# Performance work log

Measured on AMD Instinct MI355X. Metric: run time of the kernel, lower is better.

## Reference

```python
import jax, jax.numpy as jnp
import numpy as np

NUM_CLASSES = 4      # config.class_num (malaria stages)
N = 2048             # total nodes = source + target samples
S = 1024             # source_length
FEAT_IN = 25088      # VGG19 include_top=False -> 7*7*512 flattened
D_FC = 512           # Dense(512)
D_G1 = 512           # config.features_dim (GCNConv1 out)
D_G2 = 256           # config.GCN_hidderlayer_dim_num (GCNConv2 out)


def setup_inputs() -> dict:
    key = jax.random.key(0)
    ks = jax.random.split(key, 8)
    sc = lambda fan_in: np.float32(1.0 / np.sqrt(fan_in))
    return {
        "x": jax.random.normal(ks[0], (N, FEAT_IN), jnp.float32),
        "W_fc": jax.random.normal(ks[1], (FEAT_IN, D_FC), jnp.float32) * sc(FEAT_IN),
        "b_fc": jnp.zeros((D_FC,), jnp.float32),
        "W_g1": jax.random.normal(ks[2], (D_FC, D_G1), jnp.float32) * sc(D_FC),
        "b_g1": jnp.zeros((D_G1,), jnp.float32),
        "W_g2": jax.random.normal(ks[3], (D_G1, D_G2), jnp.float32) * sc(D_G1),
        "b_g2": jnp.zeros((D_G2,), jnp.float32),
        "source_labels": jax.random.randint(ks[4], (S,), 0, NUM_CLASSES),
        "source_length": S,
    }


def reference(x, W_fc, b_fc, W_g1, b_g1, W_g2, b_g2, source_labels, source_length):
    # fc after (omitted frozen) VGG19 backbone + flatten
    feats = x @ W_fc + b_fc                                   # [N, 512]

    # get_centers: per-class SUM of source features (no averaging, faithful)
    src = feats[:source_length]                               # [S, 512]
    centers = jax.ops.segment_sum(src, source_labels, num_segments=NUM_CLASSES)  # [C, 512]

    # per-target euclidean distance to each centroid + argmin
    # (argmin of squared distance == argmin of euclidean distance)
    tgt = feats[source_length:]                               # [T, 512]
    d2 = (jnp.sum(tgt * tgt, axis=1, keepdims=True)
          - 2.0 * (tgt @ centers.T)
          + jnp.sum(centers * centers, axis=1)[None, :])      # [T, C]
    target_labels = jnp.argmin(d2, axis=1)                    # [T] int

    # label-cluster graph: edge iff same label; source block forced to identity
    all_labels = jnp.concatenate([source_labels.astype(jnp.int32),
                                  target_labels.astype(jnp.int32)])
    adj = (all_labels[:, None] == all_labels[None, :]).astype(feats.dtype)  # [N, N]
    adj = adj.at[:source_length, :source_length].set(
        jnp.eye(source_length, dtype=feats.dtype))

    # add_self_loops(value=1) then symmetric gcn_filter D^-1/2 A D^-1/2
    A = adj + jnp.eye(N, dtype=feats.dtype)
    dinv = jax.lax.rsqrt(jnp.sum(A, axis=1))                  # [N]
    A_norm = dinv[:, None] * A * dinv[None, :]                # [N, N]

    # two GCN layers (spektral GCNConv: A_norm @ (X @ W) + b) with relu
    h = jax.nn.relu(A_norm @ (feats @ W_g1) + b_g1)           # [N, 512]
    h = jax.nn.relu(A_norm @ (h @ W_g2) + b_g2)               # [N, 256]
    return (h, A_norm, feats)
```

## Files before the change

kernel.cpp:

```cpp
#include <hip/hip_runtime.h>

#define NROWS 2048
#define SLEN  1024
#define FEAT  25088
#define DFC   512
#define DG1   512
#define DG2   256
#define CSPLIT 128

typedef __attribute__((ext_vector_type(8))) short short8;
typedef __attribute__((ext_vector_type(4))) float f32x4;

__device__ __forceinline__ unsigned short bfbits(float f) {
  unsigned int u = __float_as_uint(f);
  u += 0x7fffu + ((u >> 16) & 1u);
  return (unsigned short)(u >> 16);
}

__device__ __forceinline__ unsigned int cvtpk(float lo, float hi) {
  unsigned int r;
  asm("v_cvt_pk_bf16_f32 %0, %1, %2" : "=v"(r) : "v"(lo), "v"(hi));
  return r;
}

__device__ __forceinline__ void load_lds16(const void* g, void* l) {
  __builtin_amdgcn_global_load_lds(
      (const __attribute__((address_space(1))) unsigned int*)g,
      (__attribute__((address_space(3))) unsigned int*)l, 16, 0, 0);
}

__global__ void transpose_cvt_k(const float* __restrict__ src, unsigned short* __restrict__ dst,
                                int K, int Ncol) {
  __shared__ float tile[64][65];
  int kb = blockIdx.x * 64, nb = blockIdx.y * 64;
  int tx = threadIdx.x & 63, ty = threadIdx.x >> 6;
  #pragma unroll
  for (int i = ty; i < 64; i += 4)
    tile[i][tx] = src[(size_t)(kb + i) * Ncol + (nb + tx)];
  __syncthreads();
  #pragma unroll
  for (int i = ty; i < 64; i += 4)
    dst[(size_t)(nb + i) * K + (kb + tx)] = bfbits(tile[tx][i]);
}

template<bool AF32>
__global__ __launch_bounds__(256) void gemm_k(const void* __restrict__ Aptr,
    const unsigned short* __restrict__ BT, float* __restrict__ Cacc,
    int K, int Ncols, int tiles_n, int ksteps) {
  __shared__ unsigned short Al[2][128 * 64];
  __shared__ unsigned short Bl[2][128 * 64];
  int tid = threadIdx.x;
  int m0 = (blockIdx.x / tiles_n) * 128;
  int n0 = (blockIdx.x % tiles_n) * 128;
  int kbase = blockIdx.y * ksteps * 64;
  int wid = tid >> 6, lane = tid & 63;
  int wm = wid >> 1, wn = wid & 1;
  int lrow = lane & 15, lko = lane >> 4;

  f32x4 acc[4][4];
  #pragma unroll
  for (int i = 0; i < 4; i++)
    #pragma unroll
    for (int j = 0; j < 4; j++) acc[i][j] = (f32x4){0.f, 0.f, 0.f, 0.f};

  float4 pa[8];

  auto loadA_regs = [&](int k0) {
    const float* A = (const float*)Aptr;
    #pragma unroll
    for (int j = 0; j < 4; j++) {
      int ch = tid + j * 256;
      int r = ch >> 3, c = ch & 7;
      const float* g = A + (size_t)(m0 + r) * K + k0 + c * 8;
      pa[2 * j]     = *reinterpret_cast<const float4*>(g);
      pa[2 * j + 1] = *reinterpret_cast<const float4*>(g + 4);
    }
  };
  auto cvtWriteA = [&](int buf) {
    #pragma unroll
    for (int j = 0; j < 4; j++) {
      int ch = tid + j * 256;
      int r = ch >> 3, c = ch & 7;
      int p = c ^ (r & 7);
      int4 o;
      o.x = (int)cvtpk(pa[2 * j].x,     pa[2 * j].y);
      o.y = (int)cvtpk(pa[2 * j].z,     pa[2 * j].w);
      o.z = (int)cvtpk(pa[2 * j + 1].x, pa[2 * j + 1].y);
      o.w = (int)cvtpk(pa[2 * j + 1].z, pa[2 * j + 1].w);
      *reinterpret_cast<int4*>((char*)Al[buf] + r * 128 + p * 16) = o;
    }
  };
  auto stageA_lds = [&](int buf, int k0) {
    const unsigned short* A = (const unsigned short*)Aptr;
    #pragma unroll
    for (int j = 0; j < 4; j++) {
      int chb = j * 256 + wid * 64;
      int ch = chb + lane;
      int r = ch >> 3, c = (ch & 7) ^ (r & 7);
      load_lds16(A + (size_t)(m0 + r) * K + k0 + c * 8, (char*)Al[buf] + chb * 16);
    }
  };
  auto stageB = [&](int buf, int k0) {
    #pragma unroll
    for (int j = 0; j < 4; j++) {
      int chb = j * 256 + wid * 64;
      int ch = chb + lane;
      int r = ch >> 3, c = (ch & 7) ^ (r & 7);
      load_lds16(BT + (size_t)(n0 + r) * K + k0 + c * 8, (char*)Bl[buf] + chb * 16);
    }
  };

  if constexpr (AF32) { loadA_regs(kbase); cvtWriteA(0); }
  else                { stageA_lds(0, kbase); }
  stageB(0, kbase);
  __syncthreads();

  int cur = 0;
  for (int t = 0; t < ksteps; ++t) {
    int k1 = kbase + (t + 1) * 64;
    bool more = (t + 1 < ksteps);
    if (more) {
      if constexpr (AF32) loadA_regs(k1);
      else                stageA_lds(cur ^ 1, k1);
      stageB(cur ^ 1, k1);
    }
    #pragma unroll
    for (int kk = 0; kk < 2; kk++) {
      short8 af[4], bfv[4];
      #pragma unroll
      for (int mi = 0; mi < 4; mi++) {
        int R = wm * 64 + mi * 16 + lrow;
        int slot = ((kk << 2) | lko) ^ (lrow & 7);
        af[mi] = *reinterpret_cast<const short8*>((char*)Al[cur] + R * 128 + slot * 16);
      }
      #pragma unroll
      for (int ni = 0; ni < 4; ni++) {
        int R = wn * 64 + ni * 16 + lrow;
        int slot = ((kk << 2) | lko) ^ (lrow & 7);
        bfv[ni] = *reinterpret_cast<const short8*>((char*)Bl[cur] + R * 128 + slot * 16);
      }
      #pragma unroll
      for (int mi = 0; mi < 4; mi++)
        #pragma unroll
        for (int ni = 0; ni < 4; ni++)
          acc[mi][ni] = __builtin_amdgcn_mfma_f32_16x16x32_bf16(af[mi], bfv[ni], acc[mi][ni], 0, 0, 0);
    }
    if constexpr (AF32) { if (more) cvtWriteA(cur ^ 1); }
    __syncthreads();
    cur ^= 1;
  }

  #pragma unroll
  for (int mi = 0; mi < 4; mi++)
    #pragma unroll
    for (int ni = 0; ni < 4; ni++)
      #pragma unroll
      for (int r = 0; r < 4; r++) {
        int row = m0 + wm * 64 + mi * 16 + lko * 4 + r;
        int col = n0 + wn * 64 + ni * 16 + lrow;
        atomicAdd(&Cacc[(size_t)row * Ncols + col], acc[mi][ni][r]);
      }
}

__global__ void feats_fin_k(const float* __restrict__ facc, const float* __restrict__ bfc,
                            float* __restrict__ outf, unsigned short* __restrict__ outbf) {
  int i = blockIdx.y;
  int n = blockIdx.x * 256 + threadIdx.x;
  float v = facc[(size_t)i * DFC + n] + bfc[n];
  outf[(size_t)i * DFC + n] = v;
  outbf[(size_t)i * DFC + n] = bfbits(v);
}

__global__ void seg_sum_part_k(const float* __restrict__ x, const int* __restrict__ slab,
                               float* __restrict__ sxp) {
  int k4 = blockIdx.x * 256 + threadIdx.x;
  if (k4 >= FEAT / 4) return;
  int k = k4 * 4;
  int i0 = blockIdx.y * 64, i1 = i0 + 64;
  float4 a0 = {0,0,0,0}, a1 = {0,0,0,0}, a2 = {0,0,0,0}, a3 = {0,0,0,0};
  #pragma unroll 4
  for (int i = i0; i < i1; i++) {
    float4 v = *reinterpret_cast<const float4*>(x + (size_t)i * FEAT + k);
    int c = slab[i];
    float m0 = (c == 0) ? 1.f : 0.f, m1 = (c == 1) ? 1.f : 0.f;
    float m2 = (c == 2) ? 1.f : 0.f, m3 = (c == 3) ? 1.f : 0.f;
    a0.x += m0 * v.x; a0.y += m0 * v.y; a0.z += m0 * v.z; a0.w += m0 * v.w;
    a1.x += m1 * v.x; a1.y += m1 * v.y; a1.z += m1 * v.z; a1.w += m1 * v.w;
    a2.x += m2 * v.x; a2.y += m2 * v.y; a2.z += m2 * v.z; a2.w += m2 * v.w;
    a3.x += m3 * v.x; a3.y += m3 * v.y; a3.z += m3 * v.z; a3.w += m3 * v.w;
  }
  size_t base = (size_t)blockIdx.y * 4 * FEAT;
  *reinterpret_cast<float4*>(sxp + base + 0 * FEAT + k) = a0;
  *reinterpret_cast<float4*>(sxp + base + 1 * FEAT + k) = a1;
  *reinterpret_cast<float4*>(sxp + base + 2 * FEAT + k) = a2;
  *reinterpret_cast<float4*>(sxp + base + 3 * FEAT + k) = a3;
}

__global__ void seg_sum_reduce_k(const float* __restrict__ sxp, float* __restrict__ sx) {
  int k4 = blockIdx.x * 256 + threadIdx.x;
  if (k4 >= FEAT / 4) return;
  int k = k4 * 4;
  int c = blockIdx.y;
  double s0 = 0, s1 = 0, s2 = 0, s3 = 0;
  #pragma unroll
  for (int p = 0; p < 16; p++) {
    float4 v = *reinterpret_cast<const float4*>(sxp + ((size_t)p * 4 + c) * FEAT + k);
    s0 += (double)v.x; s1 += (double)v.y; s2 += (double)v.z; s3 += (double)v.w;
  }
  float4 r; r.x = (float)s0; r.y = (float)s1; r.z = (float)s2; r.w = (float)s3;
  *reinterpret_cast<float4*>(sx + (size_t)c * FEAT + k) = r;
}

__global__ void count_src_k(const int* __restrict__ slab, int* __restrict__ cnt) {
  __shared__ int c[4];
  if (threadIdx.x < 4) c[threadIdx.x] = 0;
  __syncthreads();
  for (int i = threadIdx.x; i < SLEN; i += 256) atomicAdd(&c[slab[i]], 1);
  __syncthreads();
  if (threadIdx.x < 4) cnt[threadIdx.x] = c[threadIdx.x];
}

__global__ void centers_part_k(const float* __restrict__ sx, const float* __restrict__ W,
                               double* __restrict__ cpart) {
  int n = blockIdx.x * 64 + (threadIdx.x & 63);
  int cc = threadIdx.x >> 6;
  int kb = blockIdx.y * (FEAT / CSPLIT), ke = kb + FEAT / CSPLIT;
  const float* sr = sx + (size_t)cc * FEAT;
  double acc = 0.0;
  #pragma unroll 4
  for (int k = kb; k < ke; k++)
    acc += (double)sr[k] * (double)W[(size_t)k * DFC + n];
  cpart[((size_t)blockIdx.y * 4 + cc) * DFC + n] = acc;
}

__global__ void centers_reduce_k(const double* __restrict__ cpart, const float* __restrict__ bfc,
                                 const int* __restrict__ cntsrc, float* __restrict__ Cent) {
  int idx = blockIdx.x * 256 + threadIdx.x;
  int cc = idx >> 9, n = idx & 511;
  double s = 0.0;
  #pragma unroll 4
  for (int p = 0; p < CSPLIT; p++) s += cpart[((size_t)p * 4 + cc) * DFC + n];
  Cent[idx] = (float)(s + (double)cntsrc[cc] * (double)bfc[n]);
}

__global__ void wc_k(const float* __restrict__ W, const float* __restrict__ Cent,
                     float* __restrict__ wc) {
  __shared__ float cs[4 * DFC];
  for (int i = threadIdx.x; i < 4 * DFC; i += 256) cs[i] = Cent[i];
  __syncthreads();
  int k = blockIdx.x * 256 + threadIdx.x;
  if (k >= FEAT) return;
  const float* wr = W + (size_t)k * DFC;
  double a0 = 0, a1 = 0, a2 = 0, a3 = 0;
  #pragma unroll 2
  for (int n = 0; n < DFC; n += 4) {
    float4 w4 = *reinterpret_cast<const float4*>(wr + n);
    a0 += (double)w4.x * cs[0 * DFC + n] + (double)w4.y * cs[0 * DFC + n + 1]
        + (double)w4.z * cs[0 * DFC + n + 2] + (double)w4.w * cs[0 * DFC + n + 3];
    a1 += (double)w4.x * cs[1 * DFC + n] + (double)w4.y * cs[1 * DFC + n + 1]
        + (double)w4.z * cs[1 * DFC + n + 2] + (double)w4.w * cs[1 * DFC + n + 3];
    a2 += (double)w4.x * cs[2 * DFC + n] + (double)w4.y * cs[2 * DFC + n + 1]
        + (double)w4.z * cs[2 * DFC + n + 2] + (double)w4.w * cs[2 * DFC + n + 3];
    a3 += (double)w4.x * cs[3 * DFC + n] + (double)w4.y * cs[3 * DFC + n + 1]
        + (double)w4.z * cs[3 * DFC + n + 2] + (double)w4.w * cs[3 * DFC + n + 3];
  }
  float4 r; r.x = (float)a0; r.y = (float)a1; r.z = (float)a2; r.w = (float)a3;
  *reinterpret_cast<float4*>(wc + 4 * (size_t)k) = r;
}

__global__ void kj_k(const float* __restrict__ Cent, const float* __restrict__ bfc,
                     float* __restrict__ Kj) {
  int j = threadIdx.x >> 6, lane = threadIdx.x & 63;
  float cn = 0.f, bc = 0.f;
  for (int n = lane; n < DFC; n += 64) {
    float c = Cent[j * DFC + n];
    cn += c * c; bc += bfc[n] * c;
  }
  #pragma unroll
  for (int m = 32; m >= 1; m >>= 1) { cn += __shfl_xor(cn, m); bc += __shfl_xor(bc, m); }
  if (lane == 0) Kj[j] = cn - 2.f * bc;
}

__global__ void d2_labels_k(const float* __restrict__ x, const float* __restrict__ wc,
                            const float* __restrict__ Kj, int* __restrict__ tlab) {
  int row = blockIdx.x;
  int tid = threadIdx.x;
  const float* xr = x + (size_t)(SLEN + row) * FEAT;
  double a0 = 0, a1 = 0, a2 = 0, a3 = 0;
  #pragma unroll 2
  for (int k = tid; k < FEAT; k += 256) {
    float xv = xr[k];
    float4 w4 = *reinterpret_cast<const float4*>(wc + 4 * (size_t)k);
    a0 += (double)xv * w4.x; a1 += (double)xv * w4.y;
    a2 += (double)xv * w4.z; a3 += (double)xv * w4.w;
  }
  #pragma unroll
  for (int m = 32; m >= 1; m >>= 1) {
    a0 += __shfl_xor(a0, m); a1 += __shfl_xor(a1, m);
    a2 += __shfl_xor(a2, m); a3 += __shfl_xor(a3, m);
  }
  __shared__ double s[4][4];
  int wid = tid >> 6, lane = tid & 63;
  if (lane == 0) { s[wid][0] = a0; s[wid][1] = a1; s[wid][2] = a2; s[wid][3] = a3; }
  __syncthreads();
  if (tid == 0) {
    double t0 = s[0][0] + s[1][0] + s[2][0] + s[3][0];
    double t1 = s[0][1] + s[1][1] + s[2][1] + s[3][1];
    double t2 = s[0][2] + s[1][2] + s[2][2] + s[3][2];
    double t3 = s[0][3] + s[1][3] + s[2][3] + s[3][3];
    double s0 = (double)Kj[0] - 2.0 * t0;
    double s1 = (double)Kj[1] - 2.0 * t1;
    double s2 = (double)Kj[2] - 2.0 * t2;
    double s3 = (double)Kj[3] - 2.0 * t3;
    int bi = 0; double b = s0;
    if (s1 < b) { b = s1; bi = 1; }
    if (s2 < b) { b = s2; bi = 2; }
    if (s3 < b) { b = s3; bi = 3; }
    tlab[row] = bi;
  }
}

__global__ void finalize_labels_k(const int* __restrict__ slab, const int* __restrict__ tlab,
                                  const int* __restrict__ cntsrc, int* __restrict__ alllab,
                                  float* __restrict__ dinv) {
  __shared__ int ct[4];
  if (threadIdx.x < 4) ct[threadIdx.x] = 0;
  __syncthreads();
  for (int i = threadIdx.x; i < SLEN; i += 256) atomicAdd(&ct[tlab[i]], 1);
  __syncthreads();
  for (int i = threadIdx.x; i < NROWS; i += 256) {
    int lab = (i < SLEN) ? slab[i] : tlab[i - SLEN];
    alllab[i] = lab;
    float rs = (i < SLEN) ? (2.f + (float)ct[lab])
                          : (1.f + (float)cntsrc[lab] + (float)ct[lab]);
    dinv[i] = 1.f / sqrtf(rs);
  }
}

__global__ void anorm_k(const int* __restrict__ alllab, const float* __restrict__ dinv,
                        float* __restrict__ Aout) {
  int i = blockIdx.y;
  int j0 = (blockIdx.x * 256 + threadIdx.x) * 4;
  int li = alllab[i];
  float di = dinv[i];
  int4 lj = *reinterpret_cast<const int4*>(alllab + j0);
  float4 dj = *reinterpret_cast<const float4*>(dinv + j0);
  int jj[4] = {lj.x, lj.y, lj.z, lj.w};
  float dd[4] = {dj.x, dj.y, dj.z, dj.w};
  float4 o;
  float* op = &o.x;
  #pragma unroll
  for (int e = 0; e < 4; e++) {
    int j = j0 + e;
    float v;
    if (i == j) v = 2.f * di * dd[e];
    else if (i < SLEN && j < SLEN) v = 0.f;
    else v = (li == jj[e]) ? di * dd[e] : 0.f;
    op[e] = v;
  }
  *reinterpret_cast<float4*>(Aout + (size_t)i * NROWS + j0) = o;
}

__global__ void reduce_st_k(const float* __restrict__ Xacc, const int* __restrict__ alllab,
                            const float* __restrict__ dinv, float* __restrict__ ST, int D) {
  int n = blockIdx.x * 256 + threadIdx.x;
  int i0 = blockIdx.y * 32, i1 = i0 + 32;
  float s[4] = {0, 0, 0, 0}, tt[4] = {0, 0, 0, 0};
  for (int i = i0; i < i1; ++i) {
    float v = dinv[i] * Xacc[(size_t)i * D + n];
    int lab = alllab[i];
    bool src = i < SLEN;
    #pragma unroll
    for (int c = 0; c < 4; c++) {
      s[c]  += (src && lab == c) ? v : 0.f;
      tt[c] += (!src && lab == c) ? v : 0.f;
    }
  }
  #pragma unroll
  for (int c = 0; c < 4; c++) {
    atomicAdd(&ST[c * D + n], s[c]);
    atomicAdd(&ST[(4 + c) * D + n], tt[c]);
  }
}

__global__ void apply_prop_k(const float* __restrict__ Xacc, const float* __restrict__ ST,
                             const int* __restrict__ alllab, const float* __restrict__ dinv,
                             const float* __restrict__ bias, float* __restrict__ outf,
                             unsigned short* __restrict__ outbf, int D) {
  int i = blockIdx.y;
  int n = blockIdx.x * 256 + threadIdx.x;
  float dv = dinv[i];
  int lab = alllab[i];
  float xv = Xacc[(size_t)i * D + n];
  float z;
  if (i < SLEN) z = dv * (2.f * dv * xv + ST[(4 + lab) * D + n]);
  else          z = dv * (ST[lab * D + n] + ST[(4 + lab) * D + n] + dv * xv);
  z += bias[n];
  z = fmaxf(z, 0.f);
  if (outf)  outf[(size_t)i * D + n] = z;
  if (outbf) outbf[(size_t)i * D + n] = bfbits(z);
}

extern "C" void kernel_launch(void* const* d_in, const int* in_sizes, int n_in,
                              void* d_out, int out_size, void* d_ws, size_t ws_size,
                              hipStream_t stream) {
  const float* x    = (const float*)d_in[0];
  const float* Wfc  = (const float*)d_in[1];
  const float* bfc  = (const float*)d_in[2];
  const float* Wg1  = (const float*)d_in[3];
  const float* bg1  = (const float*)d_in[4];
  const float* Wg2  = (const float*)d_in[5];
  const float* bg2  = (const float*)d_in[6];
  const int*   slab = (const int*)d_in[7];

  float* out = (float*)d_out;
  float* out_h = out;
  float* out_A = out + 524288;
  float* out_f = out + 4718592;

  char* w = (char*)d_ws;
  unsigned short* wT   = (unsigned short*)(w);
  unsigned short* g1T  = (unsigned short*)(w + 25690112);
  unsigned short* g2T  = (unsigned short*)(w + 26214400);
  float* facc          = (float*)(w + 26476544);
  unsigned short* fbf  = (unsigned short*)(w + 30670848);
  float* x1acc         = (float*)(w + 32768000);
  unsigned short* h1bf = (unsigned short*)(w + 36962304);
  float* x2acc         = (float*)(w + 39059456);
  float* sx            = (float*)(w + 41156608);
  float* Cent          = (float*)(w + 41623552);
  float* wc            = (float*)(w + 41631744);
  float* Kj            = (float*)(w + 42033152);
  int*   tlab          = (int*)(w + 42033216);
  int*   alllab        = (int*)(w + 42037312);
  float* dinv          = (float*)(w + 42045504);
  int*   cntsrc        = (int*)(w + 42053696);
  float* ST1           = (float*)(w + 42053760);
  float* ST2           = (float*)(w + 42070144);

  float*  sxp     = (float*)(w + 32768000);
  double* cpart_d = (double*)(w + 39059456);

  hipMemsetAsync(facc,  0, (size_t)NROWS * DFC * 4, stream);
  hipMemsetAsync(ST1,   0, 8 * DG1 * 4, stream);
  hipMemsetAsync(ST2,   0, 8 * DG2 * 4, stream);

  transpose_cvt_k<<<dim3(FEAT / 64, DFC / 64), 256, 0, stream>>>(Wfc, wT, FEAT, DFC);
  transpose_cvt_k<<<dim3(DFC / 64, DG1 / 64), 256, 0, stream>>>(Wg1, g1T, DFC, DG1);
  transpose_cvt_k<<<dim3(DG1 / 64, DG2 / 64), 256, 0, stream>>>(Wg2, g2T, DG1, DG2);

  gemm_k<true><<<dim3(16 * 4, 8), 256, 0, stream>>>(x, wT, facc, FEAT, DFC, 4, 49);
  feats_fin_k<<<dim3(DFC / 256, NROWS), 256, 0, stream>>>(facc, bfc, out_f, fbf);

  seg_sum_part_k<<<dim3(25, 16), 256, 0, stream>>>(x, slab, sxp);
  seg_sum_reduce_k<<<dim3(25, 4), 256, 0, stream>>>(sxp, sx);
  count_src_k<<<1, 256, 0, stream>>>(slab, cntsrc);
  centers_part_k<<<dim3(DFC / 64, CSPLIT), 256, 0, stream>>>(sx, Wfc, cpart_d);
  centers_reduce_k<<<dim3(4 * DFC / 256), 256, 0, stream>>>(cpart_d, bfc, cntsrc, Cent);
  wc_k<<<dim3(FEAT / 256), 256, 0, stream>>>(Wfc, Cent, wc);
  kj_k<<<1, 256, 0, stream>>>(Cent, bfc, Kj);
  d2_labels_k<<<dim3(NROWS - SLEN), 256, 0, stream>>>(x, wc, Kj, tlab);
  finalize_labels_k<<<1, 256, 0, stream>>>(slab, tlab, cntsrc, alllab, dinv);

  anorm_k<<<dim3(NROWS / 1024, NROWS), 256, 0, stream>>>(alllab, dinv, out_A);

  hipMemsetAsync(x1acc, 0, (size_t)NROWS * DG1 * 4, stream);
  gemm_k<false><<<dim3(16 * 4, 4), 256, 0, stream>>>(fbf, g1T, x1acc, DFC, DG1, 4, 2);
  reduce_st_k<<<dim3(DG1 / 256, 64), 256, 0, stream>>>(x1acc, alllab, dinv, ST1, DG1);
  apply_prop_k<<<dim3(DG1 / 256, NROWS), 256, 0, stream>>>(x1acc, ST1, alllab, dinv, bg1,
                                                           nullptr, h1bf, DG1);

  hipMemsetAsync(x2acc, 0, (size_t)NROWS * DG2 * 4, stream);
  gemm_k<false><<<dim3(16 * 2, 8), 256, 0, stream>>>(h1bf, g2T, x2acc, DG1, DG2, 2, 1);
  reduce_st_k<<<dim3(DG2 / 256, 64), 256, 0, stream>>>(x2acc, alllab, dinv, ST2, DG2);
  apply_prop_k<<<dim3(DG2 / 256, NROWS), 256, 0, stream>>>(x2acc, ST2, alllab, dinv, bg2,
                                                           out_h, nullptr, DG2);

  (void)in_sizes; (void)n_in; (void)out_size; (void)ws_size;
}
```

Measured before the change: 373.8 us.

## Specialize FC GEMM with 256x256 tiles, 512 threads and deeper prefetch

Replaces the templated FC GEMM with a dedicated kernel that uses 256x256 output tiles, 512 threads, BK=32 and a 16-way split-K. It prefetches A two steps ahead in registers and issues explicit waitcnt and barrier calls so global loads overlap with MFMA work. The larger tile is meant to cut repeated reads of the fp32 x matrix and of the weights, and the split-K keeps enough blocks in flight to fill the GPU. In exchange it uses far more accumulator registers, and launch_bounds(512,2) may cause spills or lower occupancy. The hand-placed wait counts are fragile if the compiler reorders the loads.

```diff
diff --git a/kernel.cpp b/kernel.cpp
--- a/kernel.cpp
+++ b/kernel.cpp
@@ -43,8 +43,119 @@
     dst[(size_t)(nb + i) * K + (kb + tx)] = bfbits(tile[tx][i]);
 }
 
-template<bool AF32>
-__global__ __launch_bounds__(256) void gemm_k(const void* __restrict__ Aptr,
+__global__ __launch_bounds__(512, 2) void gemm_fc_k(const float* __restrict__ A,
+    const unsigned short* __restrict__ BT, float* __restrict__ Cacc, int ksteps) {
+  __shared__ unsigned short Al[2][256 * 32];
+  __shared__ unsigned short Bl[2][256 * 32];
+  const int K = FEAT;
+  int tid = threadIdx.x;
+  int m0 = (blockIdx.x >> 1) * 256;
+  int n0 = (blockIdx.x & 1) * 256;
+  int kbase = blockIdx.y * ksteps * 32;
+  int wid = tid >> 6, lane = tid & 63;
+  int wm = wid >> 1, wn = wid & 1;
+  int lrow = lane & 15, lko = lane >> 4;
+
+  f32x4 acc[4][8];
+  #pragma unroll
+  for (int i = 0; i < 4; i++)
+    #pragma unroll
+    for (int j = 0; j < 8; j++) acc[i][j] = (f32x4){0.f, 0.f, 0.f, 0.f};
+
+  float4 pa[4];
+
+  auto loadA_regs = [&](int k0) {
+    #pragma unroll
+    for (int j = 0; j < 2; j++) {
+      int ch = tid + j * 512;
+      int r = ch >> 2, c = ch & 3;
+      const float* g = A + (size_t)(m0 + r) * K + k0 + c * 8;
+      pa[2 * j]     = *reinterpret_cast<const float4*>(g);
+      pa[2 * j + 1] = *reinterpret_cast<const float4*>(g + 4);
+    }
+  };
+  auto cvtWriteA = [&](int buf) {
+    #pragma unroll
+    for (int j = 0; j < 2; j++) {
+      int ch = tid + j * 512;
+      int r = ch >> 2, c = ch & 3;
+      int p = c ^ (r & 3);
+      int4 o;
+      o.x = (int)cvtpk(pa[2 * j].x,     pa[2 * j].y);
+      o.y = (int)cvtpk(pa[2 * j].z,     pa[2 * j].w);
+      o.z = (int)cvtpk(pa[2 * j + 1].x, pa[2 * j + 1].y);
+      o.w = (int)cvtpk(pa[2 * j + 1].z, pa[2 * j + 1].w);
+      *reinterpret_cast<int4*>((char*)Al[buf] + r * 64 + p * 16) = o;
+    }
+  };
+  auto stageB = [&](int buf, int k0) {
+    #pragma unroll
+    for (int j = 0; j < 2; j++) {
+      int chb = wid * 128 + j * 64;
+      int ch = chb + lane;
+      int r = ch >> 2, c = (ch & 3) ^ (r & 3);
+      load_lds16(BT + (size_t)(n0 + r) * K + k0 + c * 8, (char*)Bl[buf] + chb * 16);
+    }
+  };
+
+  loadA_regs(kbase);
+  stageB(0, kbase);
+  cvtWriteA(0);
+  loadA_regs(kbase + 32);
+  stageB(1, kbase + 32);
+  asm volatile("s_waitcnt vmcnt(6)" ::: "memory");
+  asm volatile("s_waitcnt lgkmcnt(0)" ::: "memory");
+  __builtin_amdgcn_s_barrier();
+  __builtin_amdgcn_sched_barrier(0);
+
+  int cur = 0;
+  for (int t = 0; t < ksteps; ++t) {
+    bool more1 = (t + 1 < ksteps), more2 = (t + 2 < ksteps);
+    if (more1) cvtWriteA(cur ^ 1);
+    short8 af[4], bf8[8];
+    #pragma unroll
+    for (int mi = 0; mi < 4; mi++) {
+      int R = wm * 64 + mi * 16 + lrow;
+      int p = lko ^ (R & 3);
+      af[mi] = *reinterpret_cast<const short8*>((char*)Al[cur] + R * 64 + p * 16);
+    }
+    #pragma unroll
+    for (int ni = 0; ni < 8; ni++) {
+      int R = wn * 128 + ni * 16 + lrow;
+      int p = lko ^ (R & 3);
+      bf8[ni] = *reinterpret_cast<const short8*>((char*)Bl[cur] + R * 64 + p * 16);
+    }
+    if (more2) loadA_regs(kbase + (t + 2) * 32);
+    asm volatile("s_waitcnt lgkmcnt(0)" ::: "memory");
+    __builtin_amdgcn_s_barrier();
+    __builtin_amdgcn_sched_barrier(0);
+    if (more2) stageB(cur, kbase + (t + 2) * 32);
+    #pragma unroll
+    for (int mi = 0; mi < 4; mi++)
+      #pragma unroll
+      for (int ni = 0; ni < 8; ni++)
+        acc[mi][ni] = __builtin_amdgcn_mfma_f32_16x16x32_bf16(af[mi], bf8[ni], acc[mi][ni], 0, 0, 0);
+    if (more1) {
+      if (more2) { asm volatile("s_waitcnt vmcnt(6)" ::: "memory"); }
+      else       { asm volatile("s_waitcnt vmcnt(0)" ::: "memory"); }
+      __builtin_amdgcn_sched_barrier(0);
+    }
+    cur ^= 1;
+  }
+
+  #pragma unroll
+  for (int mi = 0; mi < 4; mi++)
+    #pragma unroll
+    for (int ni = 0; ni < 8; ni++)
+      #pragma unroll
+      for (int r = 0; r < 4; r++) {
+        int row = m0 + wm * 64 + mi * 16 + lko * 4 + r;
+        int col = n0 + wn * 128 + ni * 16 + lrow;
+        atomicAdd(&Cacc[(size_t)row * DFC + col], acc[mi][ni][r]);
+      }
+}
+
+__global__ __launch_bounds__(256) void gemm_l_k(const unsigned short* __restrict__ A,
     const unsigned short* __restrict__ BT, float* __restrict__ Cacc,
     int K, int Ncols, int tiles_n, int ksteps) {
   __shared__ unsigned short Al[2][128 * 64];
@@ -63,66 +174,26 @@
     #pragma unroll
     for (int j = 0; j < 4; j++) acc[i][j] = (f32x4){0.f, 0.f, 0.f, 0.f};
 
-  float4 pa[8];
-
-  auto loadA_regs = [&](int k0) {
-    const float* A = (const float*)Aptr;
-    #pragma unroll
-    for (int j = 0; j < 4; j++) {
-      int ch = tid + j * 256;
-      int r = ch >> 3, c = ch & 7;
-      const float* g = A + (size_t)(m0 + r) * K + k0 + c * 8;
-      pa[2 * j]     = *reinterpret_cast<const float4*>(g);
-      pa[2 * j + 1] = *reinterpret_cast<const float4*>(g + 4);
-    }
-  };
-  auto cvtWriteA = [&](int buf) {
-    #pragma unroll
-    for (int j = 0; j < 4; j++) {
-      int ch = tid + j * 256;
-      int r = ch >> 3, c = ch & 7;
-      int p = c ^ (r & 7);
-      int4 o;
-      o.x = (int)cvtpk(pa[2 * j].x,     pa[2 * j].y);
-      o.y = (int)cvtpk(pa[2 * j].z,     pa[2 * j].w);
-      o.z = (int)cvtpk(pa[2 * j + 1].x, pa[2 * j + 1].y);
-      o.w = (int)cvtpk(pa[2 * j + 1].z, pa[2 * j + 1].w);
-      *reinterpret_cast<int4*>((char*)Al[buf] + r * 128 + p * 16) = o;
-    }
-  };
-  auto stageA_lds = [&](int buf, int k0) {
-    const unsigned short* A = (const unsigned short*)Aptr;
+  auto stage = [&](unsigned short (*L)[128 * 64], const unsigned short* G, int buf, int k0) {
     #pragma unroll
     for (int j = 0; j < 4; j++) {
       int chb = j * 256 + wid * 64;
       int ch = chb + lane;
       int r = ch >> 3, c = (ch & 7) ^ (r & 7);
-      load_lds16(A + (size_t)(m0 + r) * K + k0 + c * 8, (char*)Al[buf] + chb * 16);
+      load_lds16(G + (size_t)r * K + k0 + c * 8, (char*)L[buf] + chb * 16);
     }
   };
-  auto stageB = [&](int buf, int k0) {
-    #pragma unroll
-    for (int j = 0; j < 4; j++) {
-      int chb = j * 256 + wid * 64;
-      int ch = chb + lane;
-      int r = ch >> 3, c = (ch & 7) ^ (r & 7);
-      load_lds16(BT + (size_t)(n0 + r) * K + k0 + c * 8, (char*)Bl[buf] + chb * 16);
-    }
-  };
-
-  if constexpr (AF32) { loadA_regs(kbase); cvtWriteA(0); }
-  else                { stageA_lds(0, kbase); }
-  stageB(0, kbase);
+
+  stage(Al, A + (size_t)m0 * K, 0, kbase);
+  stage(Bl, BT + (size_t)n0 * K, 0, kbase);
   __syncthreads();
 
   int cur = 0;
   for (int t = 0; t < ksteps; ++t) {
-    int k1 = kbase + (t + 1) * 64;
     bool more = (t + 1 < ksteps);
     if (more) {
-      if constexpr (AF32) loadA_regs(k1);
-      else                stageA_lds(cur ^ 1, k1);
-      stageB(cur ^ 1, k1);
+      stage(Al, A + (size_t)m0 * K, cur ^ 1, kbase + (t + 1) * 64);
+      stage(Bl, BT + (size_t)n0 * K, cur ^ 1, kbase + (t + 1) * 64);
     }
     #pragma unroll
     for (int kk = 0; kk < 2; kk++) {
@@ -145,11 +216,9 @@
         for (int ni = 0; ni < 4; ni++)
           acc[mi][ni] = __builtin_amdgcn_mfma_f32_16x16x32_bf16(af[mi], bfv[ni], acc[mi][ni], 0, 0, 0);
     }
-    if constexpr (AF32) { if (more) cvtWriteA(cur ^ 1); }
     __syncthreads();
     cur ^= 1;
   }
-
   #pragma unroll
   for (int mi = 0; mi < 4; mi++)
     #pragma unroll
@@ -449,7 +518,7 @@
   transpose_cvt_k<<<dim3(DFC / 64, DG1 / 64), 256, 0, stream>>>(Wg1, g1T, DFC, DG1);
   transpose_cvt_k<<<dim3(DG1 / 64, DG2 / 64), 256, 0, stream>>>(Wg2, g2T, DG1, DG2);
 
-  gemm_k<true><<<dim3(16 * 4, 8), 256, 0, stream>>>(x, wT, facc, FEAT, DFC, 4, 49);
+  gemm_fc_k<<<dim3(16, 16), 512, 0, stream>>>(x, wT, facc, 49);
   feats_fin_k<<<dim3(DFC / 256, NROWS), 256, 0, stream>>>(facc, bfc, out_f, fbf);
 
   seg_sum_part_k<<<dim3(25, 16), 256, 0, stream>>>(x, slab, sxp);
@@ -465,13 +534,13 @@
   anorm_k<<<dim3(NROWS / 1024, NROWS), 256, 0, stream>>>(alllab, dinv, out_A);
 
   hipMemsetAsync(x1acc, 0, (size_t)NROWS * DG1 * 4, stream);
-  gemm_k<false><<<dim3(16 * 4, 4), 256, 0, stream>>>(fbf, g1T, x1acc, DFC, DG1, 4, 2);
+  gemm_l_k<<<dim3(16 * 4, 4), 256, 0, stream>>>(fbf, g1T, x1acc, DFC, DG1, 4, 2);
   reduce_st_k<<<dim3(DG1 / 256, 64), 256, 0, stream>>>(x1acc, alllab, dinv, ST1, DG1);
   apply_prop_k<<<dim3(DG1 / 256, NROWS), 256, 0, stream>>>(x1acc, ST1, alllab, dinv, bg1,
                                                            nullptr, h1bf, DG1);
 
   hipMemsetAsync(x2acc, 0, (size_t)NROWS * DG2 * 4, stream);
-  gemm_k<false><<<dim3(16 * 2, 8), 256, 0, stream>>>(h1bf, g2T, x2acc, DG1, DG2, 2, 1);
+  gemm_l_k<<<dim3(16 * 2, 8), 256, 0, stream>>>(h1bf, g2T, x2acc, DG1, DG2, 2, 1);
   reduce_st_k<<<dim3(DG2 / 256, 64), 256, 0, stream>>>(x2acc, alllab, dinv, ST2, DG2);
   apply_prop_k<<<dim3(DG2 / 256, NROWS), 256, 0, stream>>>(x2acc, ST2, alllab, dinv, bg2,
                                                            out_h, nullptr, DG2);
```

After: 356.3 us (median of 2 runs). -4.7%, faster.
